# Performance work log

Measured on AMD Instinct MI355X. Metric: run time of the kernel, lower is better.

Reference implementation:

```python
import jax, jax.numpy as jnp
import numpy as np

DIM = 768
N_HEADS = 12
HEAD_DIM = DIM // N_HEADS
SCALE = HEAD_DIM ** -0.5


def setup_inputs() -> dict:
    key = jax.random.key(0)
    ks = jax.random.split(key, 5)
    B, T = 8, 1024
    x = jax.random.normal(ks[0], (B, T, DIM), dtype=jnp.float32)
    # nn.Linear(dim, 3*dim): weight shape [3*dim, dim], bias [3*dim]
    qkv_w = jax.random.normal(ks[1], (3 * DIM, DIM), dtype=jnp.float32) * (DIM ** -0.5)
    qkv_b = jax.random.normal(ks[2], (3 * DIM,), dtype=jnp.float32) * 0.02
    proj_w = jax.random.normal(ks[3], (DIM, DIM), dtype=jnp.float32) * (DIM ** -0.5)
    proj_b = jax.random.normal(ks[4], (DIM,), dtype=jnp.float32) * 0.02
    return {"x": x, "qkv_w": qkv_w, "qkv_b": qkv_b, "proj_w": proj_w, "proj_b": proj_b}


def reference(x, qkv_w, qkv_b, proj_w, proj_b):
    B, T, D = x.shape
    # QKV projection: [B,T,3D]
    qkv = x @ qkv_w.T + qkv_b
    qkv = qkv.reshape(B, T, 3, N_HEADS, HEAD_DIM)
    qkv = jnp.transpose(qkv, (2, 0, 3, 1, 4))  # [3,B,H,T,hd]
    q, k, v = qkv[0], qkv[1], qkv[2]
    # scores [B,H,T,T]
    scores = jnp.einsum('bhqd,bhkd->bhqk', q, k) * SCALE
    attn = jax.nn.softmax(scores, axis=-1)
    out = jnp.einsum('bhqk,bhkd->bhqd', attn, v)  # [B,H,T,hd]
    out = jnp.transpose(out, (0, 2, 1, 3)).reshape(B, T, D)
    out = out @ proj_w.T + proj_b
    return out
```

## Files before the change

kernel.cpp:

```cpp
#include <hip/hip_runtime.h>

#define DEVINL __device__ __forceinline__

typedef float f32x4 __attribute__((ext_vector_type(4)));
typedef short s16x8 __attribute__((ext_vector_type(8)));
typedef short s16x4 __attribute__((ext_vector_type(4)));

DEVINL short f2bf(float f) {
  union { float f; unsigned u; } x; x.f = f;
  unsigned r = x.u + 0x7fffu + ((x.u >> 16) & 1u);
  return (short)(r >> 16);
}

#if defined(__has_builtin)
#if __has_builtin(__builtin_amdgcn_mfma_f32_16x16x16bf16_1k)
#define HAVE_MFMA16 1
#endif
#endif

DEVINL f32x4 mfma16(s16x4 a, s16x4 b, f32x4 c) {
#ifdef HAVE_MFMA16
  return __builtin_amdgcn_mfma_f32_16x16x16bf16_1k(a, b, c, 0, 0, 0);
#else
  f32x4 d;
  asm volatile("v_mfma_f32_16x16x16_bf16 %0, %1, %2, %3\n\ts_nop 7"
               : "=v"(d) : "v"(a), "v"(b), "v"(c));
  return d;
#endif
}

#define MFMA32(a, b, c) __builtin_amdgcn_mfma_f32_16x16x32_bf16((a), (b), (c), 0, 0, 0)

__global__ __launch_bounds__(256) void cast_f32_to_bf16(const float* __restrict__ in,
                                                        short* __restrict__ out, int n) {
  int i = (blockIdx.x * 256 + threadIdx.x) * 4;
  if (i >= n) return;
  f32x4 v = *(const f32x4*)(in + i);
  s16x4 o;
  o[0] = f2bf(v[0]); o[1] = f2bf(v[1]); o[2] = f2bf(v[2]); o[3] = f2bf(v[3]);
  *(s16x4*)(out + i) = o;
}

template <int EPI>
__global__ __launch_bounds__(256) void gemm_bt(const short* __restrict__ A,
                                               const short* __restrict__ Bw,
                                               const float* __restrict__ bias,
                                               short* __restrict__ o_q, short* __restrict__ o_k,
                                               short* __restrict__ o_v, float* __restrict__ o_f,
                                               int M, int N, int K, int NB) {
  __shared__ short Alds[128 * 32];
  __shared__ short Blds[128 * 32];
  const int t = threadIdx.x;
  const int w = t >> 6, ln = t & 63;
  const int wr = w >> 1, wc = w & 1;
  const int mb = blockIdx.x / NB, nb = blockIdx.x % NB;
  const int m0 = mb * 128, n0 = nb * 128;
  const int r16 = ln & 15, g = ln >> 4;
  const int arow = ln >> 2;
  const int acol = (ln & 3) * 8;

  f32x4 acc[4][4] = {};

  for (int k0 = 0; k0 < K; k0 += 32) {
    __syncthreads();
#pragma unroll
    for (int i = 0; i < 2; ++i) {
      int row = i * 64 + w * 16 + arow;
      const short* ga = A + (long)(m0 + row) * K + k0 + acol;
      __builtin_amdgcn_global_load_lds((const __attribute__((address_space(1))) void*)ga,
                                       (__attribute__((address_space(3))) void*)&Alds[(i * 4 + w) * 512],
                                       16, 0, 0);
      const short* gb = Bw + (long)(n0 + row) * K + k0 + acol;
      __builtin_amdgcn_global_load_lds((const __attribute__((address_space(1))) void*)gb,
                                       (__attribute__((address_space(3))) void*)&Blds[(i * 4 + w) * 512],
                                       16, 0, 0);
    }
    __syncthreads();
    s16x8 af[4], bfr[4];
#pragma unroll
    for (int mi = 0; mi < 4; ++mi)
      af[mi] = *(const s16x8*)&Alds[(wr * 64 + mi * 16 + r16) * 32 + g * 8];
#pragma unroll
    for (int ni = 0; ni < 4; ++ni)
      bfr[ni] = *(const s16x8*)&Blds[(wc * 64 + ni * 16 + r16) * 32 + g * 8];
#pragma unroll
    for (int mi = 0; mi < 4; ++mi)
#pragma unroll
      for (int ni = 0; ni < 4; ++ni)
        acc[mi][ni] = MFMA32(af[mi], bfr[ni], acc[mi][ni]);
  }

  if (EPI == 0) {
#pragma unroll
    for (int mi = 0; mi < 4; ++mi) {
#pragma unroll
      for (int ni = 0; ni < 4; ++ni) {
        int n = n0 + wc * 64 + ni * 16 + r16;
        float bv = bias[n];
        int which = n / 768;
        int nr = n - which * 768;
        int h = nr >> 6, d = nr & 63;
        short* dst = (which == 0) ? o_q : ((which == 1) ? o_k : o_v);
#pragma unroll
        for (int r = 0; r < 4; ++r) {
          int m = m0 + wr * 64 + mi * 16 + g * 4 + r;
          int b = m >> 10, tr = m & 1023;
          long idx = ((long)(b * 12 + h) * 1024 + tr) * 64 + d;
          dst[idx] = f2bf(acc[mi][ni][r] + bv);
        }
      }
    }
  } else {
#pragma unroll
    for (int mi = 0; mi < 4; ++mi) {
#pragma unroll
      for (int ni = 0; ni < 4; ++ni) {
        int n = n0 + wc * 64 + ni * 16 + r16;
        float bv = bias[n];
#pragma unroll
        for (int r = 0; r < 4; ++r) {
          int m = m0 + wr * 64 + mi * 16 + g * 4 + r;
          o_f[(long)m * N + n] = acc[mi][ni][r] + bv;
        }
      }
    }
  }
}

__global__ __launch_bounds__(256) void attn_kernel(const short* __restrict__ qb,
                                                   const short* __restrict__ kb,
                                                   const short* __restrict__ vb,
                                                   short* __restrict__ ao) {
  __shared__ short Qlds[64 * 72];
  __shared__ short Klds[64 * 72];
  __shared__ short Vtlds[64 * 72];
  const int t = threadIdx.x;
  const int w = t >> 6, ln = t & 63;
  const int r16 = ln & 15, g = ln >> 4;
  const int bh = blockIdx.x >> 4;
  const int qblk = blockIdx.x & 15;
  const int b = bh / 12, h = bh % 12;
  const long base = (long)bh * 1024 * 64;
  const int q0 = qblk * 64;

#pragma unroll
  for (int it = 0; it < 2; ++it) {
    int slot = it * 256 + t;
    int row = slot >> 3, d0 = (slot & 7) << 3;
    *(s16x8*)&Qlds[row * 72 + d0] = *(const s16x8*)(qb + base + (long)(q0 + row) * 64 + d0);
  }
  __syncthreads();
  s16x8 qf[2];
#pragma unroll
  for (int kh = 0; kh < 2; ++kh)
    qf[kh] = *(const s16x8*)&Qlds[(w * 16 + r16) * 72 + kh * 32 + g * 8];

  f32x4 accO[4] = {};
  float den = 0.f;
  const int vjp = t & 31, vd0 = (t >> 5) << 3;

  for (int kt = 0; kt < 16; ++kt) {
    __syncthreads();
    const short* kp = kb + base + (long)kt * 64 * 64;
#pragma unroll
    for (int it = 0; it < 2; ++it) {
      int slot = it * 256 + t;
      int row = slot >> 3, d0 = (slot & 7) << 3;
      *(s16x8*)&Klds[row * 72 + d0] = *(const s16x8*)(kp + row * 64 + d0);
    }
    const short* vp = vb + base + (long)kt * 64 * 64;
    {
      s16x8 va = *(const s16x8*)(vp + (2 * vjp) * 64 + vd0);
      s16x8 vc = *(const s16x8*)(vp + (2 * vjp + 1) * 64 + vd0);
#pragma unroll
      for (int jj = 0; jj < 8; ++jj) {
        unsigned val = (unsigned)(unsigned short)va[jj] | ((unsigned)(unsigned short)vc[jj] << 16);
        *(unsigned*)&Vtlds[(vd0 + jj) * 72 + 2 * vjp] = val;
      }
    }
    __syncthreads();

    f32x4 st[4];
#pragma unroll
    for (int mj = 0; mj < 4; ++mj) {
      s16x8 k0f = *(const s16x8*)&Klds[(mj * 16 + r16) * 72 + g * 8];
      s16x8 k1f = *(const s16x8*)&Klds[(mj * 16 + r16) * 72 + 32 + g * 8];
      f32x4 z = {};
      z = MFMA32(k0f, qf[0], z);
      z = MFMA32(k1f, qf[1], z);
      st[mj] = z;
    }
    s16x4 pt[4];
#pragma unroll
    for (int mj = 0; mj < 4; ++mj) {
#pragma unroll
      for (int r = 0; r < 4; ++r) {
        float p = __expf(st[mj][r] * 0.125f);
        den += p;
        pt[mj][r] = f2bf(p);
      }
    }
#pragma unroll
    for (int di = 0; di < 4; ++di) {
#pragma unroll
      for (int mj = 0; mj < 4; ++mj) {
        s16x4 vf = *(const s16x4*)&Vtlds[(di * 16 + r16) * 72 + mj * 16 + g * 4];
        accO[di] = mfma16(pt[mj], vf, accO[di]);
      }
    }
  }

  den += __shfl_xor(den, 16);
  den += __shfl_xor(den, 32);
  float inv[4];
#pragma unroll
  for (int r = 0; r < 4; ++r) {
    float dr = __shfl(den, g * 4 + r);
    inv[r] = 1.0f / dr;
  }
  const long orow0 = (long)b * 1024 + q0 + w * 16;
#pragma unroll
  for (int di = 0; di < 4; ++di) {
#pragma unroll
    for (int r = 0; r < 4; ++r) {
      long row = orow0 + g * 4 + r;
      ao[row * 768 + h * 64 + di * 16 + r16] = f2bf(accO[di][r] * inv[r]);
    }
  }
}

extern "C" void kernel_launch(void* const* d_in, const int* in_sizes, int n_in,
                              void* d_out, int out_size, void* d_ws, size_t ws_size,
                              hipStream_t stream) {
  const float* x      = (const float*)d_in[0];
  const float* qkv_w  = (const float*)d_in[1];
  const float* qkv_b  = (const float*)d_in[2];
  const float* proj_w = (const float*)d_in[3];
  const float* proj_b = (const float*)d_in[4];
  float* out = (float*)d_out;

  const long BT = 8192, D = 768, D3 = 2304;
  short* ws   = (short*)d_ws;
  short* xb   = ws;
  short* wqkv = xb + BT * D;
  short* wprj = wqkv + D3 * D;
  short* q    = wprj + D * D;
  short* k    = q + BT * D;
  short* v    = k + BT * D;
  short* ao   = v + BT * D;

  cast_f32_to_bf16<<<(int)(BT * D / 4 / 256), 256, 0, stream>>>(x, xb, (int)(BT * D));
  cast_f32_to_bf16<<<(int)(D3 * D / 4 / 256), 256, 0, stream>>>(qkv_w, wqkv, (int)(D3 * D));
  cast_f32_to_bf16<<<(int)(D * D / 4 / 256), 256, 0, stream>>>(proj_w, wprj, (int)(D * D));

  gemm_bt<0><<<64 * 18, 256, 0, stream>>>(xb, wqkv, qkv_b, q, k, v, nullptr,
                                          8192, 2304, 768, 18);
  attn_kernel<<<96 * 16, 256, 0, stream>>>(q, k, v, ao);
  gemm_bt<1><<<64 * 6, 256, 0, stream>>>(ao, wprj, proj_b, nullptr, nullptr, nullptr, out,
                                         8192, 768, 768, 6);
}
```

Before: 232.0 us.

## Double query rows per attention block, fuse casts, swizzle GEMM blocks across XCDs

The attention kernel now handles 128 query rows per block instead of 64. Each K/V tile loaded into LDS is reused across two query sub-tiles, which halves K/V global traffic and the V transpose work per output. The three fp32-to-bf16 cast launches are merged into one grid-stride kernel. GEMM block indices are remapped so that contiguous tiles land on the same XCD for better L2 locality. The trade-offs are higher register use in attention and half as many attention blocks (768), which may lower occupancy and parallelism.

New measurement: 207.4 us. 1.12x faster.

```diff
diff --git a/kernel.cpp b/kernel.cpp
--- a/kernel.cpp
+++ b/kernel.cpp
@@ -31,14 +31,26 @@
 
 #define MFMA32(a, b, c) __builtin_amdgcn_mfma_f32_16x16x32_bf16((a), (b), (c), 0, 0, 0)
 
-__global__ __launch_bounds__(256) void cast_f32_to_bf16(const float* __restrict__ in,
-                                                        short* __restrict__ out, int n) {
-  int i = (blockIdx.x * 256 + threadIdx.x) * 4;
-  if (i >= n) return;
-  f32x4 v = *(const f32x4*)(in + i);
-  s16x4 o;
-  o[0] = f2bf(v[0]); o[1] = f2bf(v[1]); o[2] = f2bf(v[2]); o[3] = f2bf(v[3]);
-  *(s16x4*)(out + i) = o;
+#define AS1(p) ((const __attribute__((address_space(1))) void*)(p))
+#define AS3(p) ((__attribute__((address_space(3))) void*)(p))
+
+__global__ __launch_bounds__(256) void cast3(const float* __restrict__ a,
+                                             const float* __restrict__ b,
+                                             const float* __restrict__ c,
+                                             short* __restrict__ o) {
+  const int NA = 8192 * 768, NB2 = 2304 * 768, NC = 768 * 768;
+  const int NT = (NA + NB2 + NC) / 4;
+  for (int qd = blockIdx.x * 256 + threadIdx.x; qd < NT; qd += gridDim.x * 256) {
+    int i = qd * 4;
+    const float* src; int off;
+    if (i < NA) { src = a; off = i; }
+    else if (i < NA + NB2) { src = b; off = i - NA; }
+    else { src = c; off = i - NA - NB2; }
+    f32x4 v = *(const f32x4*)(src + off);
+    s16x4 ov;
+    ov[0] = f2bf(v[0]); ov[1] = f2bf(v[1]); ov[2] = f2bf(v[2]); ov[3] = f2bf(v[3]);
+    *(s16x4*)(o + i) = ov;
+  }
 }
 
 template <int EPI>
@@ -53,7 +65,9 @@
   const int t = threadIdx.x;
   const int w = t >> 6, ln = t & 63;
   const int wr = w >> 1, wc = w & 1;
-  const int mb = blockIdx.x / NB, nb = blockIdx.x % NB;
+  const int cpx = gridDim.x >> 3;
+  const int orig = (blockIdx.x & 7) * cpx + (blockIdx.x >> 3);
+  const int mb = orig / NB, nb = orig % NB;
   const int m0 = mb * 128, n0 = nb * 128;
   const int r16 = ln & 15, g = ln >> 4;
   const int arow = ln >> 2;
@@ -67,13 +81,9 @@
     for (int i = 0; i < 2; ++i) {
       int row = i * 64 + w * 16 + arow;
       const short* ga = A + (long)(m0 + row) * K + k0 + acol;
-      __builtin_amdgcn_global_load_lds((const __attribute__((address_space(1))) void*)ga,
-                                       (__attribute__((address_space(3))) void*)&Alds[(i * 4 + w) * 512],
-                                       16, 0, 0);
+      __builtin_amdgcn_global_load_lds(AS1(ga), AS3(&Alds[(i * 4 + w) * 512]), 16, 0, 0);
       const short* gb = Bw + (long)(n0 + row) * K + k0 + acol;
-      __builtin_amdgcn_global_load_lds((const __attribute__((address_space(1))) void*)gb,
-                                       (__attribute__((address_space(3))) void*)&Blds[(i * 4 + w) * 512],
-                                       16, 0, 0);
+      __builtin_amdgcn_global_load_lds(AS1(gb), AS3(&Blds[(i * 4 + w) * 512]), 16, 0, 0);
     }
     __syncthreads();
     s16x8 af[4], bfr[4];
@@ -131,32 +141,36 @@
                                                    const short* __restrict__ kb,
                                                    const short* __restrict__ vb,
                                                    short* __restrict__ ao) {
-  __shared__ short Qlds[64 * 72];
+  __shared__ short Qlds[128 * 72];
   __shared__ short Klds[64 * 72];
   __shared__ short Vtlds[64 * 72];
   const int t = threadIdx.x;
   const int w = t >> 6, ln = t & 63;
   const int r16 = ln & 15, g = ln >> 4;
-  const int bh = blockIdx.x >> 4;
-  const int qblk = blockIdx.x & 15;
+  const int bh = blockIdx.x >> 3;
+  const int qblk = blockIdx.x & 7;
   const int b = bh / 12, h = bh % 12;
-  const long base = (long)bh * 1024 * 64;
-  const int q0 = qblk * 64;
-
-#pragma unroll
-  for (int it = 0; it < 2; ++it) {
+  const long base = (long)bh * 65536;
+  const int q0 = qblk * 128;
+
+#pragma unroll
+  for (int it = 0; it < 4; ++it) {
     int slot = it * 256 + t;
     int row = slot >> 3, d0 = (slot & 7) << 3;
     *(s16x8*)&Qlds[row * 72 + d0] = *(const s16x8*)(qb + base + (long)(q0 + row) * 64 + d0);
   }
   __syncthreads();
-  s16x8 qf[2];
-#pragma unroll
-  for (int kh = 0; kh < 2; ++kh)
-    qf[kh] = *(const s16x8*)&Qlds[(w * 16 + r16) * 72 + kh * 32 + g * 8];
-
-  f32x4 accO[4] = {};
-  float den = 0.f;
+  s16x8 qf[2][2];
+#pragma unroll
+  for (int s = 0; s < 2; ++s) {
+    int row = s * 64 + w * 16 + r16;
+#pragma unroll
+    for (int kh = 0; kh < 2; ++kh)
+      qf[s][kh] = *(const s16x8*)&Qlds[row * 72 + kh * 32 + g * 8];
+  }
+
+  f32x4 accO[2][4] = {};
+  float den[2] = {0.f, 0.f};
   const int vjp = t & 31, vd0 = (t >> 5) << 3;
 
   for (int kt = 0; kt < 16; ++kt) {
@@ -180,24 +194,30 @@
     }
     __syncthreads();
 
-    f32x4 st[4];
+    f32x4 st[2][4];
 #pragma unroll
     for (int mj = 0; mj < 4; ++mj) {
       s16x8 k0f = *(const s16x8*)&Klds[(mj * 16 + r16) * 72 + g * 8];
       s16x8 k1f = *(const s16x8*)&Klds[(mj * 16 + r16) * 72 + 32 + g * 8];
-      f32x4 z = {};
-      z = MFMA32(k0f, qf[0], z);
-      z = MFMA32(k1f, qf[1], z);
-      st[mj] = z;
-    }
-    s16x4 pt[4];
-#pragma unroll
-    for (int mj = 0; mj < 4; ++mj) {
-#pragma unroll
-      for (int r = 0; r < 4; ++r) {
-        float p = __expf(st[mj][r] * 0.125f);
-        den += p;
-        pt[mj][r] = f2bf(p);
+#pragma unroll
+      for (int s = 0; s < 2; ++s) {
+        f32x4 z = {};
+        z = MFMA32(k0f, qf[s][0], z);
+        z = MFMA32(k1f, qf[s][1], z);
+        st[s][mj] = z;
+      }
+    }
+    s16x4 pt[2][4];
+#pragma unroll
+    for (int s = 0; s < 2; ++s) {
+#pragma unroll
+      for (int mj = 0; mj < 4; ++mj) {
+#pragma unroll
+        for (int r = 0; r < 4; ++r) {
+          float p = __expf(st[s][mj][r] * 0.125f);
+          den[s] += p;
+          pt[s][mj][r] = f2bf(p);
+        }
       }
     }
 #pragma unroll
@@ -205,26 +225,31 @@
 #pragma unroll
       for (int mj = 0; mj < 4; ++mj) {
         s16x4 vf = *(const s16x4*)&Vtlds[(di * 16 + r16) * 72 + mj * 16 + g * 4];
-        accO[di] = mfma16(pt[mj], vf, accO[di]);
-      }
-    }
-  }
-
-  den += __shfl_xor(den, 16);
-  den += __shfl_xor(den, 32);
-  float inv[4];
-#pragma unroll
-  for (int r = 0; r < 4; ++r) {
-    float dr = __shfl(den, g * 4 + r);
-    inv[r] = 1.0f / dr;
-  }
-  const long orow0 = (long)b * 1024 + q0 + w * 16;
-#pragma unroll
-  for (int di = 0; di < 4; ++di) {
+        accO[0][di] = mfma16(pt[0][mj], vf, accO[0][di]);
+        accO[1][di] = mfma16(pt[1][mj], vf, accO[1][di]);
+      }
+    }
+  }
+
+#pragma unroll
+  for (int s = 0; s < 2; ++s) {
+    float dsum = den[s];
+    dsum += __shfl_xor(dsum, 16);
+    dsum += __shfl_xor(dsum, 32);
+    float inv[4];
 #pragma unroll
     for (int r = 0; r < 4; ++r) {
-      long row = orow0 + g * 4 + r;
-      ao[row * 768 + h * 64 + di * 16 + r16] = f2bf(accO[di][r] * inv[r]);
+      float dr = __shfl(dsum, g * 4 + r);
+      inv[r] = 1.0f / dr;
+    }
+    const long orow0 = (long)b * 1024 + q0 + s * 64 + w * 16;
+#pragma unroll
+    for (int di = 0; di < 4; ++di) {
+#pragma unroll
+      for (int r = 0; r < 4; ++r) {
+        long row = orow0 + g * 4 + r;
+        ao[row * 768 + h * 64 + di * 16 + r16] = f2bf(accO[s][di][r] * inv[r]);
+      }
     }
   }
 }
@@ -249,13 +274,10 @@
   short* v    = k + BT * D;
   short* ao   = v + BT * D;
 
-  cast_f32_to_bf16<<<(int)(BT * D / 4 / 256), 256, 0, stream>>>(x, xb, (int)(BT * D));
-  cast_f32_to_bf16<<<(int)(D3 * D / 4 / 256), 256, 0, stream>>>(qkv_w, wqkv, (int)(D3 * D));
-  cast_f32_to_bf16<<<(int)(D * D / 4 / 256), 256, 0, stream>>>(proj_w, wprj, (int)(D * D));
-
+  cast3<<<2048, 256, 0, stream>>>(x, qkv_w, proj_w, ws);
   gemm_bt<0><<<64 * 18, 256, 0, stream>>>(xb, wqkv, qkv_b, q, k, v, nullptr,
                                           8192, 2304, 768, 18);
-  attn_kernel<<<96 * 16, 256, 0, stream>>>(q, k, v, ao);
+  attn_kernel<<<96 * 8, 256, 0, stream>>>(q, k, v, ao);
   gemm_bt<1><<<64 * 6, 256, 0, stream>>>(ao, wprj, proj_b, nullptr, nullptr, nullptr, out,
                                          8192, 768, 768, 6);
 }
```
